# Optimization experiments

Hardware: AMD Instinct MI355X
Metric: run time of the kernel (lower is better)

The kernel has to match this reference:

```python
import jax, jax.numpy as jnp
import numpy as np

B, T_E, T_D, H = 32, 128, 128, 256  # batch, encoder len, decoder len, hidden


def lstm_scan(x, h0, c0, Wih, Whh, bih, bhh):
    """Single-layer PyTorch-style LSTM over x: [B, T, F] -> (hs, cs) each [T, B, H]."""
    bias = bih + bhh

    def step(carry, xt):
        h, c = carry
        gates = xt @ Wih.T + h @ Whh.T + bias  # [B, 4H], gate order i,f,g,o
        i, f, g, o = jnp.split(gates, 4, axis=-1)
        i = jax.nn.sigmoid(i)
        f = jax.nn.sigmoid(f)
        o = jax.nn.sigmoid(o)
        g = jnp.tanh(g)
        c = f * c + i * g
        h = o * jnp.tanh(c)
        return (h, c), (h, c)

    _, (hs, cs) = jax.lax.scan(step, (h0, c0), jnp.swapaxes(x, 0, 1))
    return hs, cs


def setup_inputs() -> dict:
    key = jax.random.key(0)
    ks = jax.random.split(key, 16)
    seq = jax.random.normal(ks[0], (B, T_E), jnp.float32)
    seq_m = jax.random.randint(ks[1], (B, 1), 1, T_E + 1)  # valid lengths in [1, T_E]
    pos = jnp.arange(T_E)[None, :]
    seq = jnp.where(pos < seq_m, seq, 0.0)  # zero-pad beyond length (drives the mask)
    target = jax.random.normal(ks[2], (B, T_D), jnp.float32)

    s = 0.1
    nrm = lambda k, shape: s * jax.random.normal(k, shape, jnp.float32)
    return dict(
        seq=seq, seq_m=seq_m, target=target,
        Wih_e=nrm(ks[3], (4 * H, 1)), Whh_e=nrm(ks[4], (4 * H, H)),
        bih_e=nrm(ks[5], (4 * H,)), bhh_e=nrm(ks[6], (4 * H,)),
        Wih_d=nrm(ks[7], (4 * H, 1)), Whh_d=nrm(ks[8], (4 * H, H)),
        bih_d=nrm(ks[9], (4 * H,)), bhh_d=nrm(ks[10], (4 * H,)),
        We=nrm(ks[11], (H, H)), be=nrm(ks[12], (H,)),
        Wd=nrm(ks[13], (H, H)), bd=nrm(ks[14], (H,)),
        v=jnp.ones((H,), jnp.float32),
    )


def reference(seq, seq_m, target,
              Wih_e, Whh_e, bih_e, bhh_e,
              Wih_d, Whh_d, bih_d, bhh_d,
              We, be, Wd, bd, v):
    zeros = jnp.zeros((B, H), seq.dtype)
    # Encoder: one fused scan instead of the original per-timestep Python loop
    hs_e, cs_e = lstm_scan(seq[..., None], zeros, zeros, Wih_e, Whh_e, bih_e, bhh_e)
    e = jnp.swapaxes(hs_e, 0, 1)  # [B, T_E, H]

    # Grab encoder state at the last valid step (seq_m - 1) per batch element
    last = seq_m[:, 0] - 1  # [B]
    bidx = jnp.arange(B)
    e_hs = hs_e[last, bidx]  # [B, H]
    e_cs = cs_e[last, bidx]

    # Decoder initialized from the selected encoder state
    hs_d, _ = lstm_scan(target[..., None], e_hs, e_cs, Wih_d, Whh_d, bih_d, bhh_d)
    d = jnp.swapaxes(hs_d, 0, 1)  # [B, T_D, H]

    e2 = e @ We.T + be  # [B, T_E, H]
    d2 = d @ Wd.T + bd  # [B, T_D, H]

    # Additive (Bahdanau) attention: tanh(e_j + d_i) . v  -> [B, T_D, T_E]
    t = jnp.tanh(d2[:, :, None, :] + e2[:, None, :, :])  # [B, T_D, T_E, H]
    p = jnp.einsum('bijh,h->bij', t, v)

    # Masking: original sets seq[:,0]=0.1 then adds 1000 where seq value nonzero,
    # after subtracting 1000 everywhere -> padded (zero) positions end up at -1000.
    seq0 = seq.at[:, 0].set(0.1)
    mask = (seq0 != 0).astype(p.dtype)  # [B, T_E]
    p = p + (mask[:, None, :] - 1.0) * 1000.0

    return jax.nn.softmax(p, axis=-1)  # pointer distribution over encoder positions
```

## Files before the change

### kernel.cpp

```cpp
#include <hip/hip_runtime.h>
#include <hip/hip_bf16.h>

#define BB 32
#define TT 128
#define HH 256
#define G4 4
#define UPB 64
#define RPB 256

#define AGENT __HIP_MEMORY_SCOPE_AGENT
#define AL(p) __hip_atomic_load((p), __ATOMIC_RELAXED, AGENT)

__device__ __forceinline__ float sigmoid_f(float x) {
    return 1.f / (1.f + __expf(-x));
}
__device__ __forceinline__ float tanh_f(float x) {
    float e = __expf(2.f * x);
    return 1.f - 2.f / (e + 1.f);
}

__global__ __launch_bounds__(256) void prep_transpose(
    const float* __restrict__ We, const float* __restrict__ Wd,
    float* __restrict__ WeT, float* __restrict__ WdT) {
    __shared__ float t[64][65];
    const int m = blockIdx.x >> 4;
    const int tile = blockIdx.x & 15;
    const float* S = m ? Wd : We;
    float* D = m ? WdT : WeT;
    const int r0 = (tile >> 2) * 64, c0 = (tile & 3) * 64;
    const int lr = threadIdx.x >> 4;
    const int lc = threadIdx.x & 15;
    for (int rr = lr; rr < 64; rr += 16)
        *(float4*)&t[rr][lc * 4] = *(const float4*)&S[(r0 + rr) * HH + c0 + lc * 4];
    __syncthreads();
    for (int rr = lr; rr < 64; rr += 16) {
        float4 v;
        v.x = t[lc * 4 + 0][rr];
        v.y = t[lc * 4 + 1][rr];
        v.z = t[lc * 4 + 2][rr];
        v.w = t[lc * 4 + 3][rr];
        *(float4*)&D[(c0 + rr) * HH + r0 + lc * 4] = v;
    }
}

__global__ __launch_bounds__(512, 2) void lstm_kernel(
    const float* __restrict__ seq,
    const int* __restrict__ seq_m,
    const float* __restrict__ target,
    const float* __restrict__ Wih_e,
    const float* __restrict__ Whh_e,
    const float* __restrict__ bih_e, const float* __restrict__ bhh_e,
    const float* __restrict__ Wih_d, const float* __restrict__ Whh_d,
    const float* __restrict__ bih_d, const float* __restrict__ bhh_d,
    float* __restrict__ e_out,
    float* __restrict__ d_out,
    unsigned long long* __restrict__ mbox,
    unsigned long long* __restrict__ hsave)
{
    const int blk = blockIdx.x;
    const int b = blk & 31;
    const int g = blk >> 5;
    const int tid = threadIdx.x;
    const int row_local = tid >> 1;
    const int half = tid & 1;
    const int gate = row_local >> 6;
    const int u_local = row_local & 63;
    const int row_global = gate * HH + g * UPB + u_local;
    const int last = seq_m[b] - 1;

    __shared__ float h_lds[HH];
    __shared__ float g_lds[RPB];
    __shared__ float x_lds[2 * TT];

    for (int i = tid; i < TT; i += 512) {
        x_lds[i] = seq[b * TT + i];
        x_lds[TT + i] = target[b * TT + i];
    }

    float4 w[32];
    float bias_r, wih_r;
    auto loadw = [&](const float* Whh, const float* Wih,
                     const float* bih, const float* bhh) {
        const float4* wr = (const float4*)(Whh + row_global * HH + half * 128);
#pragma unroll
        for (int i = 0; i < 32; ++i) w[i] = wr[i];
        bias_r = bih[row_global] + bhh[row_global];
        wih_r = Wih[row_global];
    };
    loadw(Whh_e, Wih_e, bih_e, bhh_e);

    if (tid < 64) ((float4*)h_lds)[tid] = make_float4(0.f, 0.f, 0.f, 0.f);
    __syncthreads();

    float c = 0.f, c_saved = 0.f, h_saved = 0.f;

    for (int t = 0; t < 2 * TT; ++t) {
        const int phase = t >> 7;
        const int tt = t & 127;
        const float x = x_lds[t];

        const float4* h4 = ((const float4*)h_lds) + half * 32;
        float4 a4 = make_float4(0.f, 0.f, 0.f, 0.f);
#pragma unroll
        for (int i = 0; i < 32; ++i) {
            float4 hv = h4[i];
            a4.x = fmaf(w[i].x, hv.x, a4.x);
            a4.y = fmaf(w[i].y, hv.y, a4.y);
            a4.z = fmaf(w[i].z, hv.z, a4.z);
            a4.w = fmaf(w[i].w, hv.w, a4.w);
        }
        float acc = (a4.x + a4.y) + (a4.z + a4.w);
        acc += __shfl_xor(acc, 1);
        float gv = acc + bias_r + x * wih_r;
        if (half == 0) g_lds[row_local] = gv;
        __syncthreads();

        if (tid < 64) {
            float gi = g_lds[tid];
            float gf = g_lds[64 + tid];
            float gg = g_lds[128 + tid];
            float go = g_lds[192 + tid];
            float si = sigmoid_f(gi);
            float sf = sigmoid_f(gf);
            float tg = tanh_f(gg);
            float so = sigmoid_f(go);
            c = sf * c + si * tg;
            float h = so * tanh_f(c);
            const int ug = g * UPB + tid;
            unsigned long long pkt =
                ((unsigned long long)(unsigned)(t + 1) << 32) | __float_as_uint(h);
            __hip_atomic_store(&mbox[(t & 1) * BB * HH + b * HH + ug], pkt,
                               __ATOMIC_RELAXED, AGENT);
            if (phase == 0 && tt == last) {
                c_saved = c;
                h_saved = h;
                unsigned long long spkt =
                    (1ull << 32) | (unsigned long long)__float_as_uint(h);
                __hip_atomic_store(&hsave[b * HH + ug], spkt, __ATOMIC_RELAXED, AGENT);
            }
            h_lds[ug] = (t == TT - 1) ? h_saved : h;
            (phase ? d_out : e_out)[(b * TT + tt) * HH + ug] = h;
        }

        if (tid >= 64 && tid < 256) {
            const int p = (g + (tid >> 6)) & 3;
            const int lane = tid & 63;
            const int pu = p * UPB + lane;
            unsigned long long* src;
            unsigned want;
            if (t == TT - 1) {
                src = &hsave[b * HH + pu];
                want = 1u;
            } else {
                src = &mbox[(t & 1) * BB * HH + b * HH + pu];
                want = (unsigned)(t + 1);
            }
            unsigned long long pv;
            {
                unsigned long long r0 = AL(src);
                __builtin_amdgcn_s_sleep(3);
                unsigned long long r1 = AL(src);
                __builtin_amdgcn_s_sleep(3);
                unsigned long long r2 = AL(src);
                __builtin_amdgcn_s_sleep(3);
                unsigned long long r3 = AL(src);
                for (;;) {
                    if ((unsigned)(r0 >> 32) == want) { pv = r0; break; }
                    r0 = AL(src);
                    if ((unsigned)(r1 >> 32) == want) { pv = r1; break; }
                    r1 = AL(src);
                    if ((unsigned)(r2 >> 32) == want) { pv = r2; break; }
                    r2 = AL(src);
                    if ((unsigned)(r3 >> 32) == want) { pv = r3; break; }
                    r3 = AL(src);
                }
            }
            h_lds[pu] = __uint_as_float((unsigned)pv);
        }
        __syncthreads();

        if (t == TT - 1) {
            loadw(Whh_d, Wih_d, bih_d, bhh_d);
            c = c_saved;
        }
    }
}

__global__ __launch_bounds__(256) void proj_kernel(
    const float* __restrict__ e_in, const float* __restrict__ d_in,
    const float* __restrict__ WeT, const float* __restrict__ WdT,
    const float* __restrict__ be, const float* __restrict__ bd,
    float* __restrict__ e2, float* __restrict__ d2) {
    __shared__ float tile[16][HH];
    const int blk = blockIdx.x;
    const bool isd = blk >= 256;
    const float* in = isd ? d_in : e_in;
    const float* WT = isd ? WdT : WeT;
    const float* bias = isd ? bd : be;
    float* out = isd ? d2 : e2;
    const int r0 = (isd ? blk - 256 : blk) * 16;
    const int tid = threadIdx.x;

    {
        const float4* src = (const float4*)(in + r0 * HH);
        float4* dst = (float4*)(&tile[0][0]);
        for (int idx = tid; idx < 16 * 64; idx += 256) dst[idx] = src[idx];
    }
    __syncthreads();

    float acc[16];
#pragma unroll
    for (int r = 0; r < 16; ++r) acc[r] = 0.f;
    const int cidx = tid;
    for (int k = 0; k < HH; k += 4) {
        float w0 = WT[(k + 0) * HH + cidx];
        float w1 = WT[(k + 1) * HH + cidx];
        float w2 = WT[(k + 2) * HH + cidx];
        float w3 = WT[(k + 3) * HH + cidx];
#pragma unroll
        for (int r = 0; r < 16; ++r) {
            float4 iv = *(const float4*)&tile[r][k];
            acc[r] = fmaf(iv.x, w0, acc[r]);
            acc[r] = fmaf(iv.y, w1, acc[r]);
            acc[r] = fmaf(iv.z, w2, acc[r]);
            acc[r] = fmaf(iv.w, w3, acc[r]);
        }
    }
    const float bb = bias[cidx];
#pragma unroll
    for (int r = 0; r < 16; ++r) out[(r0 + r) * HH + cidx] = acc[r] + bb;
}

#define EPAD 260
__global__ __launch_bounds__(256) void attn_kernel(
    const float* __restrict__ e2, const float* __restrict__ d2,
    const float* __restrict__ vv, const float* __restrict__ seq,
    float* __restrict__ out) {
    __shared__ float e2c[32][EPAD];
    __shared__ float d2t[8][EPAD];
    __shared__ float p_lds[8][128];
    __shared__ float v_lds[HH];

    const int blk = blockIdx.x;
    const int b = blk >> 4;
    const int i0 = (blk & 15) * 8;
    const int tid = threadIdx.x;
    const int jl = tid & 31, ii = tid >> 5;

    if (tid < 64) *(float4*)&v_lds[tid * 4] = ((const float4*)vv)[tid];
    for (int idx = tid; idx < 8 * 64; idx += 256) {
        int r = idx >> 6, q = idx & 63;
        *(float4*)&d2t[r][q * 4] = ((const float4*)(d2 + (b * TT + i0 + r) * HH))[q];
    }

    for (int jc = 0; jc < TT; jc += 32) {
        __syncthreads();
        for (int idx = tid; idx < 32 * 64; idx += 256) {
            int r = idx >> 6, q = idx & 63;
            *(float4*)&e2c[r][q * 4] = ((const float4*)(e2 + (b * TT + jc + r) * HH))[q];
        }
        __syncthreads();

        float acc = 0.f;
        for (int h = 0; h < HH; h += 4) {
            float4 ev = *(const float4*)&e2c[jl][h];
            float4 dv = *(const float4*)&d2t[ii][h];
            float4 vx = *(const float4*)&v_lds[h];
            acc = fmaf(tanh_f(ev.x + dv.x), vx.x, acc);
            acc = fmaf(tanh_f(ev.y + dv.y), vx.y, acc);
            acc = fmaf(tanh_f(ev.z + dv.z), vx.z, acc);
            acc = fmaf(tanh_f(ev.w + dv.w), vx.w, acc);
        }
        const int j = jc + jl;
        float sv = (j == 0) ? 0.1f : seq[b * TT + j];
        if (sv == 0.f) acc -= 1000.f;
        p_lds[ii][j] = acc;
    }
    __syncthreads();

    const int gr = tid >> 5, l = tid & 31;
    float x0 = p_lds[gr][l], x1 = p_lds[gr][l + 32];
    float x2 = p_lds[gr][l + 64], x3 = p_lds[gr][l + 96];
    float m = fmaxf(fmaxf(x0, x1), fmaxf(x2, x3));
#pragma unroll
    for (int o = 16; o >= 1; o >>= 1) m = fmaxf(m, __shfl_xor(m, o));
    float q0 = __expf(x0 - m), q1 = __expf(x1 - m);
    float q2 = __expf(x2 - m), q3 = __expf(x3 - m);
    float s = (q0 + q1) + (q2 + q3);
#pragma unroll
    for (int o = 16; o >= 1; o >>= 1) s += __shfl_xor(s, o);
    float inv = 1.f / s;
    float* orow = out + (b * TT + i0 + gr) * TT;
    orow[l] = q0 * inv;
    orow[l + 32] = q1 * inv;
    orow[l + 64] = q2 * inv;
    orow[l + 96] = q3 * inv;
}

extern "C" void kernel_launch(void* const* d_in, const int* in_sizes, int n_in,
                              void* d_out, int out_size, void* d_ws, size_t ws_size,
                              hipStream_t stream) {
    const float* seq = (const float*)d_in[0];
    const int* seq_m = (const int*)d_in[1];
    const float* target = (const float*)d_in[2];
    const float* Wih_e = (const float*)d_in[3];
    const float* Whh_e = (const float*)d_in[4];
    const float* bih_e = (const float*)d_in[5];
    const float* bhh_e = (const float*)d_in[6];
    const float* Wih_d = (const float*)d_in[7];
    const float* Whh_d = (const float*)d_in[8];
    const float* bih_d = (const float*)d_in[9];
    const float* bhh_d = (const float*)d_in[10];
    const float* We = (const float*)d_in[11];
    const float* be = (const float*)d_in[12];
    const float* Wd = (const float*)d_in[13];
    const float* bd = (const float*)d_in[14];
    const float* vv = (const float*)d_in[15];

    float* ws = (float*)d_ws;
    const size_t SZ_ED = (size_t)BB * TT * HH;
    float* e_buf = ws;
    float* d_buf = e_buf + SZ_ED;
    float* e2 = d_buf + SZ_ED;
    float* d2 = e2 + SZ_ED;
    float* WeT = d2 + SZ_ED;
    float* WdT = WeT + HH * HH;
    unsigned long long* mbox = (unsigned long long*)(WdT + HH * HH);
    unsigned long long* hsave = mbox + 2 * BB * HH;

    const size_t needed = (4 * SZ_ED + 2 * HH * HH) * sizeof(float) +
                          3 * BB * HH * sizeof(unsigned long long);
    if (ws_size < needed) return;

    hipMemsetAsync(mbox, 0, 3 * BB * HH * sizeof(unsigned long long), stream);
    prep_transpose<<<32, 256, 0, stream>>>(We, Wd, WeT, WdT);
    lstm_kernel<<<BB * G4, 512, 0, stream>>>(seq, seq_m, target, Wih_e, Whh_e, bih_e,
                                             bhh_e, Wih_d, Whh_d, bih_d, bhh_d, e_buf,
                                             d_buf, mbox, hsave);
    proj_kernel<<<512, 256, 0, stream>>>(e_buf, d_buf, WeT, WdT, be, bd, e2, d2);
    attn_kernel<<<512, 256, 0, stream>>>(e2, d2, vv, seq, (float*)d_out);
}
```

Before: 671.5 us.

## Use hardware reciprocal, drop spin sleeps, tile attention two decoder rows per thread

Replaces divisions in sigmoid/tanh with the hardware reciprocal instruction and removes the s_sleep calls between mailbox polls in the LSTM handoff to cut wake-up latency. The attention kernel now handles 16 decoder rows per block, two per thread, so each encoder float4 load is reused twice, and it launches half as many blocks. The softmax is reorganized for 16 lanes per row. Costs: reciprocal precision is slightly lower, polling without sleep adds memory traffic, and fewer attention blocks means less parallelism.

```diff
diff --git a/kernel.cpp b/kernel.cpp
--- a/kernel.cpp
+++ b/kernel.cpp
@@ -11,12 +11,13 @@
 #define AGENT __HIP_MEMORY_SCOPE_AGENT
 #define AL(p) __hip_atomic_load((p), __ATOMIC_RELAXED, AGENT)
 
+__device__ __forceinline__ float rcp_f(float x) { return __builtin_amdgcn_rcpf(x); }
 __device__ __forceinline__ float sigmoid_f(float x) {
-    return 1.f / (1.f + __expf(-x));
+    return rcp_f(1.f + __expf(-x));
 }
 __device__ __forceinline__ float tanh_f(float x) {
     float e = __expf(2.f * x);
-    return 1.f - 2.f / (e + 1.f);
+    return 1.f - 2.f * rcp_f(e + 1.f);
 }
 
 __global__ __launch_bounds__(256) void prep_transpose(
@@ -158,11 +159,8 @@
             unsigned long long pv;
             {
                 unsigned long long r0 = AL(src);
-                __builtin_amdgcn_s_sleep(3);
                 unsigned long long r1 = AL(src);
-                __builtin_amdgcn_s_sleep(3);
                 unsigned long long r2 = AL(src);
-                __builtin_amdgcn_s_sleep(3);
                 unsigned long long r3 = AL(src);
                 for (;;) {
                     if ((unsigned)(r0 >> 32) == want) { pv = r0; break; }
@@ -232,23 +230,24 @@
 }
 
 #define EPAD 260
+#define PPAD 132
 __global__ __launch_bounds__(256) void attn_kernel(
     const float* __restrict__ e2, const float* __restrict__ d2,
     const float* __restrict__ vv, const float* __restrict__ seq,
     float* __restrict__ out) {
     __shared__ float e2c[32][EPAD];
-    __shared__ float d2t[8][EPAD];
-    __shared__ float p_lds[8][128];
+    __shared__ float d2t[16][EPAD];
+    __shared__ float p_lds[16][PPAD];
     __shared__ float v_lds[HH];
 
     const int blk = blockIdx.x;
-    const int b = blk >> 4;
-    const int i0 = (blk & 15) * 8;
+    const int b = blk >> 3;
+    const int i0 = (blk & 7) * 16;
     const int tid = threadIdx.x;
-    const int jl = tid & 31, ii = tid >> 5;
+    const int jl = tid & 31, ig = tid >> 5;
 
     if (tid < 64) *(float4*)&v_lds[tid * 4] = ((const float4*)vv)[tid];
-    for (int idx = tid; idx < 8 * 64; idx += 256) {
+    for (int idx = tid; idx < 16 * 64; idx += 256) {
         int r = idx >> 6, q = idx & 63;
         *(float4*)&d2t[r][q * 4] = ((const float4*)(d2 + (b * TT + i0 + r) * HH))[q];
     }
@@ -261,40 +260,51 @@
         }
         __syncthreads();
 
-        float acc = 0.f;
+        float a0 = 0.f, a1 = 0.f;
         for (int h = 0; h < HH; h += 4) {
             float4 ev = *(const float4*)&e2c[jl][h];
-            float4 dv = *(const float4*)&d2t[ii][h];
             float4 vx = *(const float4*)&v_lds[h];
-            acc = fmaf(tanh_f(ev.x + dv.x), vx.x, acc);
-            acc = fmaf(tanh_f(ev.y + dv.y), vx.y, acc);
-            acc = fmaf(tanh_f(ev.z + dv.z), vx.z, acc);
-            acc = fmaf(tanh_f(ev.w + dv.w), vx.w, acc);
+            float4 d0 = *(const float4*)&d2t[ig * 2 + 0][h];
+            float4 d1 = *(const float4*)&d2t[ig * 2 + 1][h];
+            a0 = fmaf(tanh_f(ev.x + d0.x), vx.x, a0);
+            a0 = fmaf(tanh_f(ev.y + d0.y), vx.y, a0);
+            a0 = fmaf(tanh_f(ev.z + d0.z), vx.z, a0);
+            a0 = fmaf(tanh_f(ev.w + d0.w), vx.w, a0);
+            a1 = fmaf(tanh_f(ev.x + d1.x), vx.x, a1);
+            a1 = fmaf(tanh_f(ev.y + d1.y), vx.y, a1);
+            a1 = fmaf(tanh_f(ev.z + d1.z), vx.z, a1);
+            a1 = fmaf(tanh_f(ev.w + d1.w), vx.w, a1);
         }
         const int j = jc + jl;
         float sv = (j == 0) ? 0.1f : seq[b * TT + j];
-        if (sv == 0.f) acc -= 1000.f;
-        p_lds[ii][j] = acc;
+        float msk = (sv == 0.f) ? -1000.f : 0.f;
+        p_lds[ig * 2 + 0][j] = a0 + msk;
+        p_lds[ig * 2 + 1][j] = a1 + msk;
     }
     __syncthreads();
 
-    const int gr = tid >> 5, l = tid & 31;
-    float x0 = p_lds[gr][l], x1 = p_lds[gr][l + 32];
-    float x2 = p_lds[gr][l + 64], x3 = p_lds[gr][l + 96];
-    float m = fmaxf(fmaxf(x0, x1), fmaxf(x2, x3));
-#pragma unroll
-    for (int o = 16; o >= 1; o >>= 1) m = fmaxf(m, __shfl_xor(m, o));
-    float q0 = __expf(x0 - m), q1 = __expf(x1 - m);
-    float q2 = __expf(x2 - m), q3 = __expf(x3 - m);
-    float s = (q0 + q1) + (q2 + q3);
-#pragma unroll
-    for (int o = 16; o >= 1; o >>= 1) s += __shfl_xor(s, o);
-    float inv = 1.f / s;
-    float* orow = out + (b * TT + i0 + gr) * TT;
-    orow[l] = q0 * inv;
-    orow[l + 32] = q1 * inv;
-    orow[l + 64] = q2 * inv;
-    orow[l + 96] = q3 * inv;
+    const int r = tid >> 4, l16 = tid & 15;
+    float xr[8];
+    float m = -1e30f;
+#pragma unroll
+    for (int k = 0; k < 8; ++k) {
+        xr[k] = p_lds[r][l16 + 16 * k];
+        m = fmaxf(m, xr[k]);
+    }
+#pragma unroll
+    for (int o = 8; o >= 1; o >>= 1) m = fmaxf(m, __shfl_xor(m, o));
+    float s = 0.f;
+#pragma unroll
+    for (int k = 0; k < 8; ++k) {
+        xr[k] = __expf(xr[k] - m);
+        s += xr[k];
+    }
+#pragma unroll
+    for (int o = 8; o >= 1; o >>= 1) s += __shfl_xor(s, o);
+    float inv = rcp_f(s);
+    float* orow = out + (b * TT + i0 + r) * TT;
+#pragma unroll
+    for (int k = 0; k < 8; ++k) orow[l16 + 16 * k] = xr[k] * inv;
 }
 
 extern "C" void kernel_launch(void* const* d_in, const int* in_sizes, int n_in,
@@ -338,5 +348,5 @@
                                              bhh_e, Wih_d, Whh_d, bih_d, bhh_d, e_buf,
                                              d_buf, mbox, hsave);
     proj_kernel<<<512, 256, 0, stream>>>(e_buf, d_buf, WeT, WdT, be, bd, e2, d2);
-    attn_kernel<<<512, 256, 0, stream>>>(e2, d2, vv, seq, (float*)d_out);
-}
+    attn_kernel<<<BB * 8, 256, 0, stream>>>(e2, d2, vv, seq, (float*)d_out);
+}
```

Measured after the change: 687.5 us. 2.4% more time.
